# Kernel tuning notes

Hardware: AMD Instinct MI355X
Metric: run time of the kernel (lower is better)

Reference implementation:

```python
import jax, jax.numpy as jnp
import numpy as np

INP_DIM = 1024
PROJ_DIM = 1024
SEQ = 2048
BATCH = 4

def setup_inputs() -> dict:
    key = jax.random.key(0)
    k1, k2, k3, k4 = jax.random.split(key, 4)
    inputs = jax.random.normal(k1, (BATCH, SEQ, INP_DIM), dtype=jnp.float32)
    # nn.Linear weights stored as (out, in); we keep them that way and transpose in matmul
    Wq = jax.random.normal(k2, (PROJ_DIM, INP_DIM), dtype=jnp.float32) * (1.0 / np.sqrt(INP_DIM))
    Wk = jax.random.normal(k3, (PROJ_DIM, INP_DIM), dtype=jnp.float32) * (1.0 / np.sqrt(INP_DIM))
    Wv = jax.random.normal(k4, (PROJ_DIM, INP_DIM), dtype=jnp.float32) * (1.0 / np.sqrt(INP_DIM))
    return {"inputs": inputs, "Wq": Wq, "Wk": Wk, "Wv": Wv}

def reference(inputs, Wq, Wk, Wv):
    # QKV projections: x @ W.T (nn.Linear convention)
    Q = jnp.einsum('bsd,pd->bsp', inputs, Wq)
    K = jnp.einsum('bsd,pd->bsp', inputs, Wk)
    V = jnp.einsum('bsd,pd->bsp', inputs, Wv)
    scores = jnp.einsum('bqp,bkp->bqk', Q, K)  # [B, S, S]
    n = inputs.shape[1]
    causal = jnp.tril(jnp.ones((n, n), dtype=bool))  # True = keep
    scores = jnp.where(causal, scores, -jnp.inf)
    weights = jax.nn.softmax(scores / jnp.sqrt(jnp.float32(Q.shape[-1])), axis=-1)
    # dropout rate = 0.0 -> identity
    Z = jnp.einsum('bqk,bkp->bqp', weights, V)
    return Z
```

## Files before the change

kernel.cpp:

```cpp
#include <hip/hip_runtime.h>
#include <stdint.h>

#define SEQ   2048
#define DIM   1024
#define BATCH 4

typedef _Float16 f16;
typedef __attribute__((ext_vector_type(8))) _Float16 f16x8;
typedef __attribute__((ext_vector_type(4))) _Float16 f16x4;
typedef __attribute__((ext_vector_type(4))) float   f32x4;

typedef void __attribute__((address_space(1))) vg_t;
typedef void __attribute__((address_space(3))) vl_t;

__device__ __forceinline__ void gld16(const void* g, void* l) {
  __builtin_amdgcn_global_load_lds((vg_t*)g, (vl_t*)l, 16, 0, 0);
}

__global__ __launch_bounds__(256) void cvt_all(const float* __restrict__ x,
                                               const float* __restrict__ wq,
                                               const float* __restrict__ wk,
                                               const float* __restrict__ wv,
                                               f16* __restrict__ xb,
                                               f16* __restrict__ wh) {
  const int bx = blockIdx.x;
  const float* in; f16* out; int base;
  if (bx < 8192)       { in = x;  out = xb;             base = bx; }
  else if (bx < 9216)  { in = wq; out = wh;             base = bx - 8192; }
  else if (bx < 10240) { in = wk; out = wh + (1 << 20); base = bx - 9216; }
  else                 { in = wv; out = wh + (2 << 20); base = bx - 10240; }
  const long i = ((long)base * 256 + threadIdx.x) * 4;
  float4 v = *(const float4*)(in + i);
  f16x4 o = { (f16)v.x, (f16)v.y, (f16)v.z, (f16)v.w };
  *(f16x4*)(out + i) = o;
}

template <int MODE, int CAUSAL, int BK>
__global__ __launch_bounds__(256) void gemm_bt(const f16* __restrict__ A, int lda, long aOffZ,
                                               const f16* __restrict__ B, int ldb, long bOffZ,
                                               void* __restrict__ Cv, int ldc, long cOffZ,
                                               int K) {
  constexpr int CH  = BK / 8;
  constexpr int RPL = 64 / CH;
  constexpr int NL  = 32 / RPL;
  __shared__ __align__(16) f16 lA[128 * BK];
  __shared__ __align__(16) f16 lB[128 * BK];

  const int tid  = threadIdx.x;
  const int wave = tid >> 6;
  const int lane = tid & 63;

  int m0, n0, z;
  if (CAUSAL == 3) {
    const int id   = blockIdx.x;
    const int item = (id < 256) ? id : 767 - id;
    const int mt   = 15 - (item >> 5);
    const int j    = item & 31;
    m0 = mt * 128;
    n0 = (j & 7) * 128;
    z  = j >> 3;
  } else {
    m0 = blockIdx.x * 128;
    n0 = blockIdx.y * 128;
    z  = blockIdx.z;
  }

  if (CAUSAL == 1 && n0 >= m0 + 128) return;
  const int Keff = (CAUSAL >= 2) ? (m0 + 128) : K;

  const f16* Ab = A + (long)z * aOffZ + (long)m0 * lda;
  const f16* Bb = B + (long)z * bOffZ + (long)n0 * ldb;

  const int wm = (wave & 1) * 64;
  const int wn = (wave >> 1) * 64;

  f32x4 acc[4][4] = {};

  const int srow = lane / CH;
  const int sj   = lane % CH;
  const int fr   = lane & 15;
  const int fq   = lane >> 4;

  for (int kt = 0; kt < Keff; kt += BK) {
    __syncthreads();
#pragma unroll
    for (int j = 0; j < NL; ++j) {
      const int rgrp = j * 4 + wave;
      const int row  = rgrp * RPL + srow;
      const int gch  = sj ^ (row & (CH - 1));
      gld16(Ab + (long)row * lda + kt + gch * 8, (void*)(lA + rgrp * 512 + lane * 8));
      gld16(Bb + (long)row * ldb + kt + gch * 8, (void*)(lB + rgrp * 512 + lane * 8));
    }
    __syncthreads();

#pragma unroll
    for (int kk = 0; kk < BK; kk += 32) {
      f16x8 af[4], bf[4];
#pragma unroll
      for (int i = 0; i < 4; ++i) {
        const int arow = wm + i * 16 + fr;
        const int ach  = (kk / 8 + fq) ^ (arow & (CH - 1));
        af[i] = *(const f16x8*)(lA + arow * BK + ach * 8);
        const int brow = wn + i * 16 + fr;
        const int bch  = (kk / 8 + fq) ^ (brow & (CH - 1));
        bf[i] = *(const f16x8*)(lB + brow * BK + bch * 8);
      }
#pragma unroll
      for (int mi = 0; mi < 4; ++mi)
#pragma unroll
        for (int ni = 0; ni < 4; ++ni)
          acc[mi][ni] = __builtin_amdgcn_mfma_f32_16x16x32_f16(af[mi], bf[ni], acc[mi][ni], 0, 0, 0);
    }
  }

#pragma unroll
  for (int mi = 0; mi < 4; ++mi) {
    const int row = m0 + wm + mi * 16 + fq * 4;
#pragma unroll
    for (int ni = 0; ni < 4; ++ni) {
      const int col = n0 + wn + ni * 16 + fr;
      if constexpr (MODE == 0) {
        float* C = (float*)Cv + (long)z * cOffZ;
#pragma unroll
        for (int r = 0; r < 4; ++r) C[(long)(row + r) * ldc + col] = acc[mi][ni][r];
      } else if constexpr (MODE == 1) {
        f16* C = (f16*)Cv + (long)z * cOffZ;
#pragma unroll
        for (int r = 0; r < 4; ++r) C[(long)(row + r) * ldc + col] = (f16)acc[mi][ni][r];
      } else if constexpr (MODE == 2) {
        f16* C = (f16*)Cv + (long)z * cOffZ;
        f16x4 o = { (f16)acc[mi][ni][0], (f16)acc[mi][ni][1],
                    (f16)acc[mi][ni][2], (f16)acc[mi][ni][3] };
        *(f16x4*)(C + (long)col * ldc + row) = o;
      } else {
        f16* Qh  = (f16*)Cv;
        f16* Kh  = Qh + (size_t)8 * 1024 * 1024;
        f16* VTb = Kh + (size_t)8 * 1024 * 1024;
        if (col < 1024) {
#pragma unroll
          for (int r = 0; r < 4; ++r) Qh[(long)(row + r) * DIM + col] = (f16)acc[mi][ni][r];
        } else if (col < 2048) {
#pragma unroll
          for (int r = 0; r < 4; ++r) Kh[(long)(row + r) * DIM + (col - 1024)] = (f16)acc[mi][ni][r];
        } else {
          f16x4 o = { (f16)acc[mi][ni][0], (f16)acc[mi][ni][1],
                      (f16)acc[mi][ni][2], (f16)acc[mi][ni][3] };
          *(f16x4*)(VTb + (long)(col - 2048) * (BATCH * SEQ) + row) = o;
        }
      }
    }
  }
}

__global__ __launch_bounds__(256) void softmax_causal(f16* S) {
  const int q = blockIdx.x, b = blockIdx.y;
  f16* row = S + ((long)b * SEQ + q) * SEQ;
  const int tid = threadIdx.x;
  const int lane = tid & 63, wave = tid >> 6;
  const int nvalid = q + 1;

  f16x8 vv = {};
  if (tid * 8 < nvalid) vv = *(const f16x8*)(row + tid * 8);
  float v[8];
  float m = -3.0e38f;
#pragma unroll
  for (int i = 0; i < 8; ++i) {
    const int k = tid * 8 + i;
    v[i] = (k < nvalid) ? (float)vv[i] * 0.03125f : -3.0e38f;
    m = fmaxf(m, v[i]);
  }
#pragma unroll
  for (int off = 32; off; off >>= 1) m = fmaxf(m, __shfl_xor(m, off));
  __shared__ float redm[4], reds[4];
  if (lane == 0) redm[wave] = m;
  __syncthreads();
  m = fmaxf(fmaxf(redm[0], redm[1]), fmaxf(redm[2], redm[3]));

  float s = 0.f;
#pragma unroll
  for (int i = 0; i < 8; ++i) {
    const float p = (v[i] > -1.0e37f) ? __expf(v[i] - m) : 0.f;
    v[i] = p;
    s += p;
  }
#pragma unroll
  for (int off = 32; off; off >>= 1) s += __shfl_xor(s, off);
  if (lane == 0) reds[wave] = s;
  __syncthreads();
  s = reds[0] + reds[1] + reds[2] + reds[3];
  const float inv = 1.f / s;
  f16x8 o;
#pragma unroll
  for (int i = 0; i < 8; ++i) o[i] = (f16)(v[i] * inv);
  *(f16x8*)(row + tid * 8) = o;
}

extern "C" void kernel_launch(void* const* d_in, const int* in_sizes, int n_in,
                              void* d_out, int out_size, void* d_ws, size_t ws_size,
                              hipStream_t stream) {
  const float* x  = (const float*)d_in[0];
  const float* Wq = (const float*)d_in[1];
  const float* Wk = (const float*)d_in[2];
  const float* Wv = (const float*)d_in[3];
  float* out = (float*)d_out;

  if (ws_size < (size_t)51 * 1024 * 1024 * 2) return;

  f16* xb = (f16*)d_ws;
  f16* Wh = xb + (size_t)8 * 1024 * 1024;
  f16* Qh = Wh + (size_t)3 * 1024 * 1024;
  f16* Kh = Qh + (size_t)8 * 1024 * 1024;
  f16* VT = Kh + (size_t)8 * 1024 * 1024;
  f16* Sc = VT + (size_t)8 * 1024 * 1024;

  const long QOFF = (long)SEQ * DIM;
  const long SOFF = (long)SEQ * SEQ;

  cvt_all<<<11264, 256, 0, stream>>>(x, Wq, Wk, Wv, xb, Wh);

  gemm_bt<3, 0, 64><<<dim3(64, 24, 1), 256, 0, stream>>>(xb, DIM, 0, Wh, DIM, 0, Qh, 0, 0, DIM);

  gemm_bt<1, 1, 64><<<dim3(16, 16, 4), 256, 0, stream>>>(Qh, DIM, QOFF, Kh, DIM, QOFF,
                                                         Sc, SEQ, SOFF, DIM);

  softmax_causal<<<dim3(SEQ, BATCH), 256, 0, stream>>>(Sc);

  gemm_bt<0, 3, 64><<<dim3(512, 1, 1), 256, 0, stream>>>(Sc, SEQ, SOFF,
                                                         VT, BATCH * SEQ, SEQ,
                                                         out, DIM, (long)SEQ * DIM, SEQ);
}
```

Before: 255.1 us.

## Use 128x96 compacted causal score tiles, trim softmax writes, widen PV k-tile

Replaces the 16x16x4 grid of 128x128 score tiles (which launched then exited empty upper-triangle blocks) with a compact 748-block launch of 128x96 tiles enumerated over the causal region, using a BK of 128. Softmax now stores only up to the 128-aligned causal bound that the PV GEMM reads. The PV GEMM moves to BK=128 to halve the number of k-iterations and barriers. The risks are higher LDS use per block (56KB and 64KB), which lowers occupancy, and extra loop logic to decode the tile index.

```diff
diff --git a/kernel.cpp b/kernel.cpp
--- a/kernel.cpp
+++ b/kernel.cpp
@@ -152,12 +152,104 @@
   }
 }
 
+__global__ __launch_bounds__(256) void scores_96(const f16* __restrict__ Qh,
+                                                 const f16* __restrict__ Kh,
+                                                 f16* __restrict__ Sc) {
+  __shared__ __align__(16) f16 lA[128 * 128];
+  __shared__ __align__(16) f16 lB[96 * 128];
+
+  const int tid  = threadIdx.x;
+  const int wave = tid >> 6;
+  const int lane = tid & 63;
+  const int srow = lane >> 4;
+  const int sj   = lane & 15;
+  const int fr   = lane & 15;
+  const int fq   = lane >> 4;
+  const int wm   = (wave & 1) * 64;
+  const int wn   = (wave >> 1) * 48;
+
+  const int b = blockIdx.x;
+  const int z = b / 187;
+  int rem = b - z * 187;
+  int mt = 0;
+  while (true) {
+    const int c = (128 * mt + 127) / 96 + 1;
+    if (rem < c) break;
+    rem -= c;
+    ++mt;
+  }
+  const int m0 = mt * 128;
+  const int n0 = rem * 96;
+
+  const f16* Ab = Qh + (long)z * (SEQ * DIM) + (long)m0 * DIM;
+  const f16* Bb = Kh + (long)z * (SEQ * DIM) + (long)n0 * DIM;
+
+  f32x4 acc[4][3] = {};
+
+  for (int kt = 0; kt < DIM; kt += 128) {
+    __syncthreads();
+#pragma unroll
+    for (int j = 0; j < 8; ++j) {
+      const int rgrp = j * 4 + wave;
+      const int row  = rgrp * 4 + srow;
+      const int gch  = sj ^ (row & 15);
+      gld16(Ab + (long)row * DIM + kt + gch * 8, (void*)(lA + rgrp * 512 + lane * 8));
+    }
+#pragma unroll
+    for (int j = 0; j < 6; ++j) {
+      const int rgrp = j * 4 + wave;
+      const int row  = rgrp * 4 + srow;
+      const int gch  = sj ^ (row & 15);
+      gld16(Bb + (long)row * DIM + kt + gch * 8, (void*)(lB + rgrp * 512 + lane * 8));
+    }
+    __syncthreads();
+
+#pragma unroll
+    for (int kk = 0; kk < 128; kk += 32) {
+      f16x8 af[4], bf[3];
+#pragma unroll
+      for (int i = 0; i < 4; ++i) {
+        const int arow = wm + i * 16 + fr;
+        const int ach  = (kk / 8 + fq) ^ (arow & 15);
+        af[i] = *(const f16x8*)(lA + arow * 128 + ach * 8);
+      }
+#pragma unroll
+      for (int i = 0; i < 3; ++i) {
+        const int brow = wn + i * 16 + fr;
+        const int bch  = (kk / 8 + fq) ^ (brow & 15);
+        bf[i] = *(const f16x8*)(lB + brow * 128 + bch * 8);
+      }
+#pragma unroll
+      for (int mi = 0; mi < 4; ++mi)
+#pragma unroll
+        for (int ni = 0; ni < 3; ++ni)
+          acc[mi][ni] = __builtin_amdgcn_mfma_f32_16x16x32_f16(af[mi], bf[ni], acc[mi][ni], 0, 0, 0);
+    }
+  }
+
+  f16* C = Sc + (long)z * SEQ * SEQ;
+#pragma unroll
+  for (int mi = 0; mi < 4; ++mi) {
+    const int row = m0 + wm + mi * 16 + fq * 4;
+#pragma unroll
+    for (int ni = 0; ni < 3; ++ni) {
+      const int col = n0 + wn + ni * 16 + fr;
+      if (col < SEQ) {
+#pragma unroll
+        for (int r = 0; r < 4; ++r)
+          C[(long)(row + r) * SEQ + col] = (f16)acc[mi][ni][r];
+      }
+    }
+  }
+}
+
 __global__ __launch_bounds__(256) void softmax_causal(f16* S) {
   const int q = blockIdx.x, b = blockIdx.y;
   f16* row = S + ((long)b * SEQ + q) * SEQ;
   const int tid = threadIdx.x;
   const int lane = tid & 63, wave = tid >> 6;
   const int nvalid = q + 1;
+  const int kneed  = ((q >> 7) + 1) << 7;
 
   f16x8 vv = {};
   if (tid * 8 < nvalid) vv = *(const f16x8*)(row + tid * 8);
@@ -192,7 +284,7 @@
   f16x8 o;
 #pragma unroll
   for (int i = 0; i < 8; ++i) o[i] = (f16)(v[i] * inv);
-  *(f16x8*)(row + tid * 8) = o;
+  if (tid * 8 < kneed) *(f16x8*)(row + tid * 8) = o;
 }
 
 extern "C" void kernel_launch(void* const* d_in, const int* in_sizes, int n_in,
@@ -213,19 +305,17 @@
   f16* VT = Kh + (size_t)8 * 1024 * 1024;
   f16* Sc = VT + (size_t)8 * 1024 * 1024;
 
-  const long QOFF = (long)SEQ * DIM;
   const long SOFF = (long)SEQ * SEQ;
 
   cvt_all<<<11264, 256, 0, stream>>>(x, Wq, Wk, Wv, xb, Wh);
 
   gemm_bt<3, 0, 64><<<dim3(64, 24, 1), 256, 0, stream>>>(xb, DIM, 0, Wh, DIM, 0, Qh, 0, 0, DIM);
 
-  gemm_bt<1, 1, 64><<<dim3(16, 16, 4), 256, 0, stream>>>(Qh, DIM, QOFF, Kh, DIM, QOFF,
-                                                         Sc, SEQ, SOFF, DIM);
+  scores_96<<<748, 256, 0, stream>>>(Qh, Kh, Sc);
 
   softmax_causal<<<dim3(SEQ, BATCH), 256, 0, stream>>>(Sc);
 
-  gemm_bt<0, 3, 64><<<dim3(512, 1, 1), 256, 0, stream>>>(Sc, SEQ, SOFF,
-                                                         VT, BATCH * SEQ, SEQ,
-                                                         out, DIM, (long)SEQ * DIM, SEQ);
-}
+  gemm_bt<0, 3, 128><<<dim3(512, 1, 1), 256, 0, stream>>>(Sc, SEQ, SOFF,
+                                                          VT, BATCH * SEQ, SEQ,
+                                                          out, DIM, (long)SEQ * DIM, SEQ);
+}
```

Result: faster. 238.1 us (-6.7%).
